# Kernel tuning notes

Hardware: AMD Instinct MI355X
Metric: run time of the kernel (lower is better)

The kernel has to match this reference:

```python
import jax, jax.numpy as jnp
import numpy as np

B, A, F = 8192, 8, 256      # batch, n_agents, per-agent obs feature dim
NA = 16                     # n_actions per agent
H1, H2 = 1024, 1024
OBS_D = A * F               # 2048 flattened obs dim
ACT_D = A * NA              # 128 joint action dim
IN_D = OBS_D + ACT_D        # 2176 MLP input dim


def setup_inputs() -> dict:
    key = jax.random.key(0)
    ks = jax.random.split(key, 8)
    s = 0.02
    return {
        "obs": jax.random.normal(ks[0], (B, A, F), dtype=jnp.float32),
        "all_actions": jax.random.uniform(ks[1], (B, ACT_D), dtype=jnp.float32),
        # per-agent stacked MLP params (agent axis first)
        "W1": jax.random.normal(ks[2], (A, IN_D, H1), dtype=jnp.float32) * s,
        "b1": jnp.zeros((A, H1), dtype=jnp.float32),
        "W2": jax.random.normal(ks[3], (A, H1, H2), dtype=jnp.float32) * s,
        "b2": jnp.zeros((A, H2), dtype=jnp.float32),
        "W3": jax.random.normal(ks[4], (A, H2, NA), dtype=jnp.float32) * s,
        "b3": jnp.zeros((A, NA), dtype=jnp.float32),
    }


def reference(obs, all_actions, W1, b1, W2, b2, W3, b3):
    b_s = obs.shape[0]
    obs_flat = obs.reshape(b_s, OBS_D)                      # [B, A*F]
    # mask[a, g] = 0 on agent a's own action block, 1 elsewhere
    mask = 1.0 - jnp.repeat(jnp.eye(A, dtype=obs.dtype), NA, axis=1)  # [A, A*NA]
    # split W1 into obs / action columns (equivalent to concat-then-dense)
    W1o = W1[:, :OBS_D, :]                                  # [A, OBS_D, H1]
    W1a = W1[:, OBS_D:, :]                                  # [A, ACT_D, H1]
    h1 = jax.nn.relu(
        jnp.einsum("bd,adh->bah", obs_flat, W1o)
        + jnp.einsum("bg,ag,agh->bah", all_actions, mask, W1a)
        + b1
    )                                                        # [B, A, H1]
    h2 = jax.nn.relu(jnp.einsum("bah,ahk->bak", h1, W2) + b2)  # [B, A, H2]
    out = jnp.einsum("bak,akn->ban", h2, W3) + b3              # [B, A, NA]
    return out.reshape(b_s, A * NA)
```

## Files before the change

kernel.cpp:

```cpp
#include <hip/hip_runtime.h>
#include <hip/hip_bf16.h>
#include <cstdint>
#include <cstddef>

typedef __bf16 bf16;
typedef __attribute__((ext_vector_type(8))) __bf16 bf16x8;
typedef __attribute__((ext_vector_type(4))) float f32x4;
typedef __attribute__((ext_vector_type(4))) int i32x4;
typedef __attribute__((address_space(3))) const bf16* lds_cp;

#define B_SZ  8192
#define NAGENT 8
#define NA_N  16
#define OBS_DD 2048
#define ACT_DD 128
#define IN_DD 2176
#define H1_D  1024
#define H2_D  1024

#define BM 256
#define BN 256
#define BK 64
#define GRID_M (B_SZ / BM)
#define GRID_N (1024 / BN)

__device__ __forceinline__ void gload16(const void* g, void* l) {
    __builtin_amdgcn_global_load_lds(
        (__attribute__((address_space(1))) void*)(g),
        (__attribute__((address_space(3))) void*)(l), 16, 0, 0);
}

__global__ void k_prep(const float* __restrict__ obs, const float* __restrict__ act,
                       bf16* __restrict__ xb, const float* __restrict__ b3,
                       float* __restrict__ out, const float* __restrict__ W3,
                       bf16* __restrict__ w3t) {
    const int NX = B_SZ * (IN_DD / 8);
    const int NO = B_SZ * 128 / 4;
    const int NW3 = NAGENT * NA_N * H2_D;
    int idx = blockIdx.x * blockDim.x + threadIdx.x;
    if (idx < NX) {
        const int chunks = IN_DD / 8;
        int b = idx / chunks;
        int c8 = idx - b * chunks;
        const float* src = (c8 < OBS_DD / 8)
            ? (obs + (size_t)b * OBS_DD + c8 * 8)
            : (act + (size_t)b * ACT_DD + (c8 - OBS_DD / 8) * 8);
        float4 v0 = ((const float4*)src)[0];
        float4 v1 = ((const float4*)src)[1];
        bf16x8 o;
        o[0] = (bf16)v0.x; o[1] = (bf16)v0.y; o[2] = (bf16)v0.z; o[3] = (bf16)v0.w;
        o[4] = (bf16)v1.x; o[5] = (bf16)v1.y; o[6] = (bf16)v1.z; o[7] = (bf16)v1.w;
        ((bf16x8*)(xb + (size_t)b * IN_DD))[c8] = o;
    } else if (idx < NX + NO) {
        int i = idx - NX;
        int c = (i & 31) * 4;
        float4 v = make_float4(b3[c], b3[c + 1], b3[c + 2], b3[c + 3]);
        ((float4*)out)[i] = v;
    } else if (idx < NX + NO + NW3) {
        int i = idx - NX - NO;
        int a = i / (NA_N * H2_D);
        int n = (i / H2_D) % NA_N;
        int k = i % H2_D;
        w3t[i] = (bf16)W3[(size_t)a * H2_D * NA_N + (size_t)k * NA_N + n];
    }
}

__global__ void k_transpose_w(const float* __restrict__ src, bf16* __restrict__ dst,
                              int K, int H, int maskStart) {
    __shared__ float tile[32][33];
    int a = blockIdx.z;
    int k0 = blockIdx.x * 32, h0 = blockIdx.y * 32;
    const float* s = src + (size_t)a * K * H;
    bf16* d = dst + (size_t)a * K * H;
    int tx = threadIdx.x, ty = threadIdx.y;
    #pragma unroll
    for (int i = 0; i < 32; i += 8) {
        int k = k0 + ty + i;
        float v = s[(size_t)k * H + h0 + tx];
        if (k >= maskStart) {
            int g = k - maskStart;
            if ((g >> 4) == a) v = 0.f;
        }
        tile[ty + i][tx] = v;
    }
    __syncthreads();
    #pragma unroll
    for (int i = 0; i < 32; i += 8) {
        d[(size_t)(h0 + ty + i) * K + k0 + tx] = (bf16)tile[tx][ty + i];
    }
}

#define DSR4(d0, d1, d2, d3, addr, O0, O1, O2, O3)                      \
    asm volatile("ds_read_b128 %0, %4 offset:" #O0 "\n\t"               \
                 "ds_read_b128 %1, %4 offset:" #O1 "\n\t"               \
                 "ds_read_b128 %2, %4 offset:" #O2 "\n\t"               \
                 "ds_read_b128 %3, %4 offset:" #O3                      \
                 : "=&v"(d0), "=&v"(d1), "=&v"(d2), "=&v"(d3)           \
                 : "v"(addr))

#define BC(x) __builtin_bit_cast(bf16x8, x)

template<int FUSE>
__global__ __launch_bounds__(512, 1)
void k_gemm256(const bf16* __restrict__ Ain, size_t aStride, int lda,
               const bf16* __restrict__ Bw, const float* __restrict__ bias,
               bf16* __restrict__ Cout, size_t cStride, int K,
               int aOff, int nwg, int iters,
               const bf16* __restrict__ W3Tp, float* __restrict__ outp) {
    extern __shared__ bf16 lds[];

    const int tid = threadIdx.x;
    const int w = tid >> 6;
    const int l = tid & 63;

    const int wr = (w >> 2) * 128;
    const int wc = (w & 3) * 64;
    const int lr = l & 15;
    const int lq = l >> 4;

    const int rowA = (wr + lr) * BK;
    const int rowB = (wc + lr) * BK;
    const int ck0 = ((lq ^ (lr & 7)) * 8);
    const int ck1 = (((4 + lq) ^ (lr & 7)) * 8);

    const int sRow = w * 16 + (l >> 3);
    const int sCol = ((l & 7) ^ (l >> 3)) * 8;
    const size_t l8a = (size_t)8 * lda;
    const size_t l8b = (size_t)8 * K;

    const int nkt = K / BK;
    const int q8 = nwg >> 3;

    i32x4 ra0, ra1, ra2, ra3;
    i32x4 rb0, rb1, rb2, rb3;
    i32x4 rc0, rc1, rc2, rc3;
    i32x4 rd0, rd1, rd2, rd3;
    i32x4 re0, re1, re2, re3;
    i32x4 rf0, rf1, rf2, rf3;

#define STAGE_A(t1, half) do {                                              \
        const bf16* g_ = ((half) ? pA1 : pA0) + (t1) * BK;                  \
        bf16* d_ = &lds[(((t1) & 1) * 16384) + (half) * 8192 + w * 1024];   \
        gload16(g_, d_);                                                    \
        gload16(g_ + l8a, d_ + 512);                                        \
    } while (0)
#define STAGE_B(t2, half) do {                                              \
        const bf16* g_ = ((half) ? pB1 : pB0) + (t2) * BK;                  \
        bf16* d_ = &lds[32768 + (((t2) & 1) * 16384) + (half) * 8192 + w * 1024]; \
        gload16(g_, d_);                                                    \
        gload16(g_ + l8b, d_ + 512);                                        \
    } while (0)

#define MFMA16(ACC0, A0, A1, A2, A3, B0, B1, B2, B3)                        \
    do {                                                                    \
        acc[ACC0+0][0] = __builtin_amdgcn_mfma_f32_16x16x32_bf16(BC(A0), BC(B0), acc[ACC0+0][0], 0, 0, 0); \
        acc[ACC0+1][0] = __builtin_amdgcn_mfma_f32_16x16x32_bf16(BC(A1), BC(B0), acc[ACC0+1][0], 0, 0, 0); \
        acc[ACC0+2][0] = __builtin_amdgcn_mfma_f32_16x16x32_bf16(BC(A2), BC(B0), acc[ACC0+2][0], 0, 0, 0); \
        acc[ACC0+3][0] = __builtin_amdgcn_mfma_f32_16x16x32_bf16(BC(A3), BC(B0), acc[ACC0+3][0], 0, 0, 0); \
        acc[ACC0+0][1] = __builtin_amdgcn_mfma_f32_16x16x32_bf16(BC(A0), BC(B1), acc[ACC0+0][1], 0, 0, 0); \
        acc[ACC0+1][1] = __builtin_amdgcn_mfma_f32_16x16x32_bf16(BC(A1), BC(B1), acc[ACC0+1][1], 0, 0, 0); \
        acc[ACC0+2][1] = __builtin_amdgcn_mfma_f32_16x16x32_bf16(BC(A2), BC(B1), acc[ACC0+2][1], 0, 0, 0); \
        acc[ACC0+3][1] = __builtin_amdgcn_mfma_f32_16x16x32_bf16(BC(A3), BC(B1), acc[ACC0+3][1], 0, 0, 0); \
        acc[ACC0+0][2] = __builtin_amdgcn_mfma_f32_16x16x32_bf16(BC(A0), BC(B2), acc[ACC0+0][2], 0, 0, 0); \
        acc[ACC0+1][2] = __builtin_amdgcn_mfma_f32_16x16x32_bf16(BC(A1), BC(B2), acc[ACC0+1][2], 0, 0, 0); \
        acc[ACC0+2][2] = __builtin_amdgcn_mfma_f32_16x16x32_bf16(BC(A2), BC(B2), acc[ACC0+2][2], 0, 0, 0); \
        acc[ACC0+3][2] = __builtin_amdgcn_mfma_f32_16x16x32_bf16(BC(A3), BC(B2), acc[ACC0+3][2], 0, 0, 0); \
        acc[ACC0+0][3] = __builtin_amdgcn_mfma_f32_16x16x32_bf16(BC(A0), BC(B3), acc[ACC0+0][3], 0, 0, 0); \
        acc[ACC0+1][3] = __builtin_amdgcn_mfma_f32_16x16x32_bf16(BC(A1), BC(B3), acc[ACC0+1][3], 0, 0, 0); \
        acc[ACC0+2][3] = __builtin_amdgcn_mfma_f32_16x16x32_bf16(BC(A2), BC(B3), acc[ACC0+2][3], 0, 0, 0); \
        acc[ACC0+3][3] = __builtin_amdgcn_mfma_f32_16x16x32_bf16(BC(A3), BC(B3), acc[ACC0+3][3], 0, 0, 0); \
    } while (0)

    for (int it = 0; it < iters; ++it) {
        const int b = blockIdx.x + gridDim.x * it;
        const int lin2 = (b & 7) * q8 + (b >> 3);
        const int mt = lin2 % GRID_M;
        const int rest = lin2 / GRID_M;
        const int ntile = rest % GRID_N;
        const int az = rest / GRID_N;
        const int aw = az + aOff;

        const int rowBase = mt * BM;
        const int colBase = ntile * BN;
        const bf16* Aag = Ain + (size_t)az * aStride;
        const bf16* Bag = Bw + (size_t)aw * (size_t)1024 * K;

        const bf16* pA0 = Aag + (size_t)(rowBase + sRow) * lda + sCol;
        const bf16* pA1 = Aag + (size_t)(rowBase + 128 + sRow) * lda + sCol;
        const bf16* pB0 = Bag + (size_t)(colBase + sRow) * K + sCol;
        const bf16* pB1 = Bag + (size_t)(colBase + 128 + sRow) * K + sCol;

        f32x4 acc[8][4] = {};

        STAGE_A(0, 0); STAGE_A(0, 1);
        STAGE_B(0, 0); STAGE_B(0, 1);
        asm volatile("s_waitcnt vmcnt(0)" ::: "memory");
        __builtin_amdgcn_s_barrier();

        for (int t = 0; t < nkt; ++t) {
            const int dbuf = (t & 1) * 16384;
            lds_cp adrA0 = (lds_cp)lds + (dbuf + rowA + ck0);
            lds_cp adrA1 = (lds_cp)lds + (dbuf + rowA + ck1);
            lds_cp adrB0 = (lds_cp)lds + (32768 + dbuf + rowB + ck0);
            lds_cp adrB1 = (lds_cp)lds + (32768 + dbuf + rowB + ck1);

            DSR4(ra0, ra1, ra2, ra3, adrA0, 0, 2048, 4096, 6144);
            DSR4(rb0, rb1, rb2, rb3, adrB0, 0, 2048, 4096, 6144);
            DSR4(rc0, rc1, rc2, rc3, adrA0, 8192, 10240, 12288, 14336);
            DSR4(rd0, rd1, rd2, rd3, adrB1, 0, 2048, 4096, 6144);

            if (t + 1 < nkt) {
                STAGE_A(t + 1, 0); STAGE_A(t + 1, 1);
                STAGE_B(t + 1, 0); STAGE_B(t + 1, 1);
            }

            asm volatile("s_waitcnt lgkmcnt(8)" ::: "memory");
            __builtin_amdgcn_sched_barrier(0);
            __builtin_amdgcn_s_setprio(1);
            MFMA16(0, ra0, ra1, ra2, ra3, rb0, rb1, rb2, rb3);
            __builtin_amdgcn_s_setprio(0);

            DSR4(re0, re1, re2, re3, adrA1, 0, 2048, 4096, 6144);
            asm volatile("s_waitcnt lgkmcnt(4)" ::: "memory");
            __builtin_amdgcn_sched_barrier(0);
            __builtin_amdgcn_s_setprio(1);
            MFMA16(4, rc0, rc1, rc2, rc3, rb0, rb1, rb2, rb3);
            __builtin_amdgcn_s_setprio(0);

            DSR4(rf0, rf1, rf2, rf3, adrA1, 8192, 10240, 12288, 14336);
            asm volatile("s_waitcnt lgkmcnt(4)" ::: "memory");
            __builtin_amdgcn_sched_barrier(0);
            __builtin_amdgcn_s_setprio(1);
            MFMA16(0, re0, re1, re2, re3, rd0, rd1, rd2, rd3);
            __builtin_amdgcn_s_setprio(0);

            asm volatile("s_waitcnt vmcnt(0)" ::: "memory");
            asm volatile("s_waitcnt lgkmcnt(0)" ::: "memory");
            __builtin_amdgcn_sched_barrier(0);
            __builtin_amdgcn_s_setprio(1);
            MFMA16(4, rf0, rf1, rf2, rf3, rd0, rd1, rd2, rd3);
            __builtin_amdgcn_s_setprio(0);

            __builtin_amdgcn_s_barrier();
        }

        __syncthreads();
        const float* bAg = bias + (size_t)aw * 1024;
        float bb4[4];
        #pragma unroll
        for (int n = 0; n < 4; ++n) bb4[n] = bAg[colBase + wc + n * 16 + lr];
        #pragma unroll
        for (int m = 0; m < 8; ++m)
            #pragma unroll
            for (int n = 0; n < 4; ++n)
                #pragma unroll
                for (int r = 0; r < 4; ++r) {
                    float v = acc[m][n][r] + bb4[n];
                    v = fmaxf(v, 0.f);
                    int row = wr + m * 16 + lq * 4 + r;
                    int col = wc + n * 16 + lr;
                    lds[row * 256 + ((((col >> 3) ^ (row & 7)) << 3) | (col & 7))] = (bf16)v;
                }
        __syncthreads();

        if constexpr (!FUSE) {
            bf16* Cg = Cout + (size_t)az * cStride + (size_t)rowBase * 1024 + colBase;
            const int er = tid >> 5;
            const int ec = tid & 31;
            #pragma unroll
            for (int i = 0; i < 16; ++i) {
                int row = i * 16 + er;
                int phys = ec ^ (row & 7);
                *(bf16x8*)&Cg[(size_t)row * 1024 + ec * 8] =
                    *(const bf16x8*)&lds[row * 256 + phys * 8];
            }
        } else {
            const bf16* w3a = W3Tp + (size_t)aw * NA_N * H2_D;
            f32x4 oacc[2] = {};
            const int frow0 = w * 32;
            #pragma unroll
            for (int ks = 0; ks < 8; ++ks) {
                bf16x8 bfrag = *(const bf16x8*)&w3a[(size_t)lr * H2_D + colBase + ks * 32 + lq * 8];
                #pragma unroll
                for (int mm = 0; mm < 2; ++mm) {
                    int row = frow0 + mm * 16 + lr;
                    int lc = (ks * 4 + lq) ^ (row & 7);
                    bf16x8 afrag = *(const bf16x8*)&lds[row * 256 + lc * 8];
                    oacc[mm] = __builtin_amdgcn_mfma_f32_16x16x32_bf16(afrag, bfrag, oacc[mm], 0, 0, 0);
                }
            }
            #pragma unroll
            for (int mm = 0; mm < 2; ++mm)
                #pragma unroll
                for (int r = 0; r < 4; ++r)
                    atomicAdd(&outp[(size_t)(rowBase + frow0 + mm * 16 + lq * 4 + r) * 128
                                    + aw * NA_N + lr], oacc[mm][r]);
        }

        __syncthreads();
    }
#undef STAGE_A
#undef STAGE_B
#undef MFMA16
}

extern "C" void kernel_launch(void* const* d_in, const int* in_sizes, int n_in,
                              void* d_out, int out_size, void* d_ws, size_t ws_size,
                              hipStream_t stream) {
    const float* obs = (const float*)d_in[0];
    const float* act = (const float*)d_in[1];
    const float* W1 = (const float*)d_in[2];
    const float* b1 = (const float*)d_in[3];
    const float* W2 = (const float*)d_in[4];
    const float* b2 = (const float*)d_in[5];
    const float* W3 = (const float*)d_in[6];
    const float* b3 = (const float*)d_in[7];
    float* out = (float*)d_out;

    const size_t SZ_XB  = (size_t)B_SZ * IN_DD * 2;
    const size_t SZ_W1T = (size_t)NAGENT * H1_D * IN_DD * 2;
    const size_t SZ_W2T = (size_t)NAGENT * H1_D * H2_D * 2;
    const size_t SZ_W3T = (size_t)NAGENT * NA_N * H2_D * 2;
    const size_t SZ_H1  = (size_t)B_SZ * H1_D * 2;
    const size_t SZ_FIX = SZ_XB + SZ_W1T + SZ_W2T + SZ_W3T;

    char* ws = (char*)d_ws;
    bf16* Xb  = (bf16*)ws;
    bf16* W1T = (bf16*)(ws + SZ_XB);
    bf16* W2T = (bf16*)(ws + SZ_XB + SZ_W1T);
    bf16* W3T = (bf16*)(ws + SZ_XB + SZ_W1T + SZ_W2T);
    char* hbase = ws + SZ_FIX;

    int G = 8;
    while (G > 1 && ws_size < SZ_FIX + (size_t)G * SZ_H1) G >>= 1;

    (void)hipFuncSetAttribute((const void*)k_gemm256<0>,
                              hipFuncAttributeMaxDynamicSharedMemorySize, 131072);
    (void)hipFuncSetAttribute((const void*)k_gemm256<1>,
                              hipFuncAttributeMaxDynamicSharedMemorySize, 131072);

    {
        const int NX = B_SZ * (IN_DD / 8);
        const int NO = B_SZ * 128 / 4;
        const int NW3 = NAGENT * NA_N * H2_D;
        int n = NX + NO + NW3;
        k_prep<<<(n + 255) / 256, 256, 0, stream>>>(obs, act, Xb, b3, out, W3, W3T);
    }
    k_transpose_w<<<dim3(IN_DD / 32, H1_D / 32, NAGENT), dim3(32, 8), 0, stream>>>(
        W1, W1T, IN_DD, H1_D, OBS_DD);
    k_transpose_w<<<dim3(H1_D / 32, H2_D / 32, NAGENT), dim3(32, 8), 0, stream>>>(
        W2, W2T, H1_D, H2_D, 1 << 30);

    const size_t agElems = (size_t)B_SZ * H1_D;
    bf16* h1 = (bf16*)hbase;

    for (int g0 = 0; g0 < NAGENT; g0 += G) {
        const int nwg = 128 * G;
        const int grd = (nwg >= 256) ? 256 : nwg;
        const int iters = nwg / grd;
        k_gemm256<0><<<grd, 512, 131072, stream>>>(
            Xb, 0, IN_DD, W1T, b1, h1, agElems, IN_DD, g0, nwg, iters, nullptr, nullptr);
        k_gemm256<1><<<grd, 512, 131072, stream>>>(
            h1, agElems, H1_D, W2T, b2, nullptr, 0, H1_D, g0, nwg, iters, W3T, out);
    }
    (void)in_sizes; (void)n_in; (void)out_size;
}
```

Measured before the change: 508.2 us.

## Replace persistent GEMM loop with full grid launch and merge weight transposes

The GEMM kernels drop the persistent loop that capped the grid at 256 workgroups, each iterating over several tiles. They now launch one workgroup per output tile on a 3D grid, with the same XCD-aware tile remapping. The two weight-transpose kernels are merged into one launch, with W2 blocks exiting early when past their K range. This trades persistent-block reuse for hardware scheduling of more workgroups and one fewer launch, and adds wasted early-exit blocks in the transpose.

```diff
diff --git a/kernel.cpp b/kernel.cpp
--- a/kernel.cpp
+++ b/kernel.cpp
@@ -61,17 +61,23 @@
         int a = i / (NA_N * H2_D);
         int n = (i / H2_D) % NA_N;
         int k = i % H2_D;
-        w3t[i] = (bf16)W3[(size_t)a * H2_D * NA_N + (size_t)k * NA_N + n];
-    }
-}
-
-__global__ void k_transpose_w(const float* __restrict__ src, bf16* __restrict__ dst,
-                              int K, int H, int maskStart) {
+        w3t[i] = (bf16)W3[(size_t)a * H2_D * NAGENT * 0 + (size_t)a * H2_D * NA_N + (size_t)k * NA_N + n];
+    }
+}
+
+__global__ void k_transpose_w12(const float* __restrict__ W1, bf16* __restrict__ W1T,
+                                const float* __restrict__ W2, bf16* __restrict__ W2T) {
     __shared__ float tile[32][33];
-    int a = blockIdx.z;
+    const int z = blockIdx.z;
+    const bool isW1 = (z < 8);
+    const int a = isW1 ? z : z - 8;
+    const int K = isW1 ? IN_DD : H1_D;
+    const int H = 1024;
+    const int maskStart = isW1 ? OBS_DD : (1 << 30);
+    if (!isW1 && blockIdx.x >= (H1_D / 32)) return;
+    const float* s = (isW1 ? W1 : W2) + (size_t)a * K * H;
+    bf16* d = (isW1 ? W1T : W2T) + (size_t)a * K * H;
     int k0 = blockIdx.x * 32, h0 = blockIdx.y * 32;
-    const float* s = src + (size_t)a * K * H;
-    bf16* d = dst + (size_t)a * K * H;
     int tx = threadIdx.x, ty = threadIdx.y;
     #pragma unroll
     for (int i = 0; i < 32; i += 8) {
@@ -105,13 +111,27 @@
 void k_gemm256(const bf16* __restrict__ Ain, size_t aStride, int lda,
                const bf16* __restrict__ Bw, const float* __restrict__ bias,
                bf16* __restrict__ Cout, size_t cStride, int K,
-               int aOff, int nwg, int iters,
+               int aOff, int gridZ,
                const bf16* __restrict__ W3Tp, float* __restrict__ outp) {
     extern __shared__ bf16 lds[];
 
     const int tid = threadIdx.x;
     const int w = tid >> 6;
     const int l = tid & 63;
+
+    int flat = blockIdx.x + GRID_M * (blockIdx.y + GRID_N * blockIdx.z);
+    int q8 = (GRID_M * GRID_N * gridZ) >> 3;
+    int lin2 = (flat & 7) * q8 + (flat >> 3);
+    const int mt = lin2 % GRID_M;
+    int rest = lin2 / GRID_M;
+    const int ntile = rest % GRID_N;
+    const int az = rest / GRID_N;
+    const int aw = az + aOff;
+
+    const int rowBase = mt * BM;
+    const int colBase = ntile * BN;
+    const bf16* Aag = Ain + (size_t)az * aStride;
+    const bf16* Bag = Bw + (size_t)aw * (size_t)1024 * K;
 
     const int wr = (w >> 2) * 128;
     const int wc = (w & 3) * 64;
@@ -125,18 +145,14 @@
 
     const int sRow = w * 16 + (l >> 3);
     const int sCol = ((l & 7) ^ (l >> 3)) * 8;
+    const bf16* pA0 = Aag + (size_t)(rowBase + sRow) * lda + sCol;
+    const bf16* pA1 = Aag + (size_t)(rowBase + 128 + sRow) * lda + sCol;
+    const bf16* pB0 = Bag + (size_t)(colBase + sRow) * K + sCol;
+    const bf16* pB1 = Bag + (size_t)(colBase + 128 + sRow) * K + sCol;
     const size_t l8a = (size_t)8 * lda;
     const size_t l8b = (size_t)8 * K;
 
     const int nkt = K / BK;
-    const int q8 = nwg >> 3;
-
-    i32x4 ra0, ra1, ra2, ra3;
-    i32x4 rb0, rb1, rb2, rb3;
-    i32x4 rc0, rc1, rc2, rc3;
-    i32x4 rd0, rd1, rd2, rd3;
-    i32x4 re0, re1, re2, re3;
-    i32x4 rf0, rf1, rf2, rf3;
 
 #define STAGE_A(t1, half) do {                                              \
         const bf16* g_ = ((half) ? pA1 : pA0) + (t1) * BK;                  \
@@ -150,6 +166,14 @@
         gload16(g_, d_);                                                    \
         gload16(g_ + l8b, d_ + 512);                                        \
     } while (0)
+
+    f32x4 acc[8][4] = {};
+    i32x4 ra0, ra1, ra2, ra3;
+    i32x4 rb0, rb1, rb2, rb3;
+    i32x4 rc0, rc1, rc2, rc3;
+    i32x4 rd0, rd1, rd2, rd3;
+    i32x4 re0, re1, re2, re3;
+    i32x4 rf0, rf1, rf2, rf3;
 
 #define MFMA16(ACC0, A0, A1, A2, A3, B0, B1, B2, B3)                        \
     do {                                                                    \
@@ -171,137 +195,113 @@
         acc[ACC0+3][3] = __builtin_amdgcn_mfma_f32_16x16x32_bf16(BC(A3), BC(B3), acc[ACC0+3][3], 0, 0, 0); \
     } while (0)
 
-    for (int it = 0; it < iters; ++it) {
-        const int b = blockIdx.x + gridDim.x * it;
-        const int lin2 = (b & 7) * q8 + (b >> 3);
-        const int mt = lin2 % GRID_M;
-        const int rest = lin2 / GRID_M;
-        const int ntile = rest % GRID_N;
-        const int az = rest / GRID_N;
-        const int aw = az + aOff;
-
-        const int rowBase = mt * BM;
-        const int colBase = ntile * BN;
-        const bf16* Aag = Ain + (size_t)az * aStride;
-        const bf16* Bag = Bw + (size_t)aw * (size_t)1024 * K;
-
-        const bf16* pA0 = Aag + (size_t)(rowBase + sRow) * lda + sCol;
-        const bf16* pA1 = Aag + (size_t)(rowBase + 128 + sRow) * lda + sCol;
-        const bf16* pB0 = Bag + (size_t)(colBase + sRow) * K + sCol;
-        const bf16* pB1 = Bag + (size_t)(colBase + 128 + sRow) * K + sCol;
-
-        f32x4 acc[8][4] = {};
-
-        STAGE_A(0, 0); STAGE_A(0, 1);
-        STAGE_B(0, 0); STAGE_B(0, 1);
+    STAGE_A(0, 0); STAGE_A(0, 1);
+    STAGE_B(0, 0); STAGE_B(0, 1);
+    asm volatile("s_waitcnt vmcnt(0)" ::: "memory");
+    __builtin_amdgcn_s_barrier();
+
+    for (int t = 0; t < nkt; ++t) {
+        const int dbuf = (t & 1) * 16384;
+        lds_cp adrA0 = (lds_cp)lds + (dbuf + rowA + ck0);
+        lds_cp adrA1 = (lds_cp)lds + (dbuf + rowA + ck1);
+        lds_cp adrB0 = (lds_cp)lds + (32768 + dbuf + rowB + ck0);
+        lds_cp adrB1 = (lds_cp)lds + (32768 + dbuf + rowB + ck1);
+
+        DSR4(ra0, ra1, ra2, ra3, adrA0, 0, 2048, 4096, 6144);
+        DSR4(rb0, rb1, rb2, rb3, adrB0, 0, 2048, 4096, 6144);
+        DSR4(rc0, rc1, rc2, rc3, adrA0, 8192, 10240, 12288, 14336);
+        DSR4(rd0, rd1, rd2, rd3, adrB1, 0, 2048, 4096, 6144);
+
+        if (t + 1 < nkt) {
+            STAGE_A(t + 1, 0); STAGE_A(t + 1, 1);
+            STAGE_B(t + 1, 0); STAGE_B(t + 1, 1);
+        }
+
+        asm volatile("s_waitcnt lgkmcnt(8)" ::: "memory");
+        __builtin_amdgcn_sched_barrier(0);
+        __builtin_amdgcn_s_setprio(1);
+        MFMA16(0, ra0, ra1, ra2, ra3, rb0, rb1, rb2, rb3);
+        __builtin_amdgcn_s_setprio(0);
+
+        DSR4(re0, re1, re2, re3, adrA1, 0, 2048, 4096, 6144);
+        asm volatile("s_waitcnt lgkmcnt(4)" ::: "memory");
+        __builtin_amdgcn_sched_barrier(0);
+        __builtin_amdgcn_s_setprio(1);
+        MFMA16(4, rc0, rc1, rc2, rc3, rb0, rb1, rb2, rb3);
+        __builtin_amdgcn_s_setprio(0);
+
+        DSR4(rf0, rf1, rf2, rf3, adrA1, 8192, 10240, 12288, 14336);
+        asm volatile("s_waitcnt lgkmcnt(4)" ::: "memory");
+        __builtin_amdgcn_sched_barrier(0);
+        __builtin_amdgcn_s_setprio(1);
+        MFMA16(0, re0, re1, re2, re3, rd0, rd1, rd2, rd3);
+        __builtin_amdgcn_s_setprio(0);
+
         asm volatile("s_waitcnt vmcnt(0)" ::: "memory");
+        asm volatile("s_waitcnt lgkmcnt(0)" ::: "memory");
+        __builtin_amdgcn_sched_barrier(0);
+        __builtin_amdgcn_s_setprio(1);
+        MFMA16(4, rf0, rf1, rf2, rf3, rd0, rd1, rd2, rd3);
+        __builtin_amdgcn_s_setprio(0);
+
         __builtin_amdgcn_s_barrier();
-
-        for (int t = 0; t < nkt; ++t) {
-            const int dbuf = (t & 1) * 16384;
-            lds_cp adrA0 = (lds_cp)lds + (dbuf + rowA + ck0);
-            lds_cp adrA1 = (lds_cp)lds + (dbuf + rowA + ck1);
-            lds_cp adrB0 = (lds_cp)lds + (32768 + dbuf + rowB + ck0);
-            lds_cp adrB1 = (lds_cp)lds + (32768 + dbuf + rowB + ck1);
-
-            DSR4(ra0, ra1, ra2, ra3, adrA0, 0, 2048, 4096, 6144);
-            DSR4(rb0, rb1, rb2, rb3, adrB0, 0, 2048, 4096, 6144);
-            DSR4(rc0, rc1, rc2, rc3, adrA0, 8192, 10240, 12288, 14336);
-            DSR4(rd0, rd1, rd2, rd3, adrB1, 0, 2048, 4096, 6144);
-
-            if (t + 1 < nkt) {
-                STAGE_A(t + 1, 0); STAGE_A(t + 1, 1);
-                STAGE_B(t + 1, 0); STAGE_B(t + 1, 1);
-            }
-
-            asm volatile("s_waitcnt lgkmcnt(8)" ::: "memory");
-            __builtin_amdgcn_sched_barrier(0);
-            __builtin_amdgcn_s_setprio(1);
-            MFMA16(0, ra0, ra1, ra2, ra3, rb0, rb1, rb2, rb3);
-            __builtin_amdgcn_s_setprio(0);
-
-            DSR4(re0, re1, re2, re3, adrA1, 0, 2048, 4096, 6144);
-            asm volatile("s_waitcnt lgkmcnt(4)" ::: "memory");
-            __builtin_amdgcn_sched_barrier(0);
-            __builtin_amdgcn_s_setprio(1);
-            MFMA16(4, rc0, rc1, rc2, rc3, rb0, rb1, rb2, rb3);
-            __builtin_amdgcn_s_setprio(0);
-
-            DSR4(rf0, rf1, rf2, rf3, adrA1, 8192, 10240, 12288, 14336);
-            asm volatile("s_waitcnt lgkmcnt(4)" ::: "memory");
-            __builtin_amdgcn_sched_barrier(0);
-            __builtin_amdgcn_s_setprio(1);
-            MFMA16(0, re0, re1, re2, re3, rd0, rd1, rd2, rd3);
-            __builtin_amdgcn_s_setprio(0);
-
-            asm volatile("s_waitcnt vmcnt(0)" ::: "memory");
-            asm volatile("s_waitcnt lgkmcnt(0)" ::: "memory");
-            __builtin_amdgcn_sched_barrier(0);
-            __builtin_amdgcn_s_setprio(1);
-            MFMA16(4, rf0, rf1, rf2, rf3, rd0, rd1, rd2, rd3);
-            __builtin_amdgcn_s_setprio(0);
-
-            __builtin_amdgcn_s_barrier();
-        }
-
-        __syncthreads();
-        const float* bAg = bias + (size_t)aw * 1024;
-        float bb4[4];
-        #pragma unroll
-        for (int n = 0; n < 4; ++n) bb4[n] = bAg[colBase + wc + n * 16 + lr];
-        #pragma unroll
-        for (int m = 0; m < 8; ++m)
-            #pragma unroll
-            for (int n = 0; n < 4; ++n)
-                #pragma unroll
-                for (int r = 0; r < 4; ++r) {
-                    float v = acc[m][n][r] + bb4[n];
-                    v = fmaxf(v, 0.f);
-                    int row = wr + m * 16 + lq * 4 + r;
-                    int col = wc + n * 16 + lr;
-                    lds[row * 256 + ((((col >> 3) ^ (row & 7)) << 3) | (col & 7))] = (bf16)v;
-                }
-        __syncthreads();
-
-        if constexpr (!FUSE) {
-            bf16* Cg = Cout + (size_t)az * cStride + (size_t)rowBase * 1024 + colBase;
-            const int er = tid >> 5;
-            const int ec = tid & 31;
-            #pragma unroll
-            for (int i = 0; i < 16; ++i) {
-                int row = i * 16 + er;
-                int phys = ec ^ (row & 7);
-                *(bf16x8*)&Cg[(size_t)row * 1024 + ec * 8] =
-                    *(const bf16x8*)&lds[row * 256 + phys * 8];
-            }
-        } else {
-            const bf16* w3a = W3Tp + (size_t)aw * NA_N * H2_D;
-            f32x4 oacc[2] = {};
-            const int frow0 = w * 32;
-            #pragma unroll
-            for (int ks = 0; ks < 8; ++ks) {
-                bf16x8 bfrag = *(const bf16x8*)&w3a[(size_t)lr * H2_D + colBase + ks * 32 + lq * 8];
-                #pragma unroll
-                for (int mm = 0; mm < 2; ++mm) {
-                    int row = frow0 + mm * 16 + lr;
-                    int lc = (ks * 4 + lq) ^ (row & 7);
-                    bf16x8 afrag = *(const bf16x8*)&lds[row * 256 + lc * 8];
-                    oacc[mm] = __builtin_amdgcn_mfma_f32_16x16x32_bf16(afrag, bfrag, oacc[mm], 0, 0, 0);
-                }
-            }
-            #pragma unroll
-            for (int mm = 0; mm < 2; ++mm)
-                #pragma unroll
-                for (int r = 0; r < 4; ++r)
-                    atomicAdd(&outp[(size_t)(rowBase + frow0 + mm * 16 + lq * 4 + r) * 128
-                                    + aw * NA_N + lr], oacc[mm][r]);
-        }
-
-        __syncthreads();
     }
 #undef STAGE_A
 #undef STAGE_B
 #undef MFMA16
+
+    __syncthreads();
+    const float* bAg = bias + (size_t)aw * 1024;
+    float bb4[4];
+    #pragma unroll
+    for (int n = 0; n < 4; ++n) bb4[n] = bAg[colBase + wc + n * 16 + lr];
+    #pragma unroll
+    for (int m = 0; m < 8; ++m)
+        #pragma unroll
+        for (int n = 0; n < 4; ++n)
+            #pragma unroll
+            for (int r = 0; r < 4; ++r) {
+                float v = acc[m][n][r] + bb4[n];
+                v = fmaxf(v, 0.f);
+                int row = wr + m * 16 + lq * 4 + r;
+                int col = wc + n * 16 + lr;
+                lds[row * 256 + ((((col >> 3) ^ (row & 7)) << 3) | (col & 7))] = (bf16)v;
+            }
+    __syncthreads();
+
+    if constexpr (!FUSE) {
+        bf16* Cg = Cout + (size_t)az * cStride + (size_t)rowBase * 1024 + colBase;
+        const int er = tid >> 5;
+        const int ec = tid & 31;
+        #pragma unroll
+        for (int i = 0; i < 16; ++i) {
+            int row = i * 16 + er;
+            int phys = ec ^ (row & 7);
+            *(bf16x8*)&Cg[(size_t)row * 1024 + ec * 8] =
+                *(const bf16x8*)&lds[row * 256 + phys * 8];
+        }
+    } else {
+        const bf16* w3a = W3Tp + (size_t)aw * NA_N * H2_D;
+        f32x4 oacc[2] = {};
+        const int frow0 = w * 32;
+        #pragma unroll
+        for (int ks = 0; ks < 8; ++ks) {
+            bf16x8 bfrag = *(const bf16x8*)&w3a[(size_t)lr * H2_D + colBase + ks * 32 + lq * 8];
+            #pragma unroll
+            for (int mm = 0; mm < 2; ++mm) {
+                int row = frow0 + mm * 16 + lr;
+                int lc = (ks * 4 + lq) ^ (row & 7);
+                bf16x8 afrag = *(const bf16x8*)&lds[row * 256 + lc * 8];
+                oacc[mm] = __builtin_amdgcn_mfma_f32_16x16x32_bf16(afrag, bfrag, oacc[mm], 0, 0, 0);
+            }
+        }
+        #pragma unroll
+        for (int mm = 0; mm < 2; ++mm)
+            #pragma unroll
+            for (int r = 0; r < 4; ++r)
+                atomicAdd(&outp[(size_t)(rowBase + frow0 + mm * 16 + lq * 4 + r) * 128
+                                + aw * NA_N + lr], oacc[mm][r]);
+    }
 }
 
 extern "C" void kernel_launch(void* const* d_in, const int* in_sizes, int n_in,
@@ -346,22 +346,17 @@
         int n = NX + NO + NW3;
         k_prep<<<(n + 255) / 256, 256, 0, stream>>>(obs, act, Xb, b3, out, W3, W3T);
     }
-    k_transpose_w<<<dim3(IN_DD / 32, H1_D / 32, NAGENT), dim3(32, 8), 0, stream>>>(
-        W1, W1T, IN_DD, H1_D, OBS_DD);
-    k_transpose_w<<<dim3(H1_D / 32, H2_D / 32, NAGENT), dim3(32, 8), 0, stream>>>(
-        W2, W2T, H1_D, H2_D, 1 << 30);
+    k_transpose_w12<<<dim3(IN_DD / 32, 1024 / 32, 16), dim3(32, 8), 0, stream>>>(
+        W1, W1T, W2, W2T);
 
     const size_t agElems = (size_t)B_SZ * H1_D;
     bf16* h1 = (bf16*)hbase;
 
     for (int g0 = 0; g0 < NAGENT; g0 += G) {
-        const int nwg = 128 * G;
-        const int grd = (nwg >= 256) ? 256 : nwg;
-        const int iters = nwg / grd;
-        k_gemm256<0><<<grd, 512, 131072, stream>>>(
-            Xb, 0, IN_DD, W1T, b1, h1, agElems, IN_DD, g0, nwg, iters, nullptr, nullptr);
-        k_gemm256<1><<<grd, 512, 131072, stream>>>(
-            h1, agElems, H1_D, W2T, b2, nullptr, 0, H1_D, g0, nwg, iters, W3T, out);
+        k_gemm256<0><<<dim3(GRID_M, GRID_N, G), 512, 131072, stream>>>(
+            Xb, 0, IN_DD, W1T, b1, h1, agElems, IN_DD, g0, G, nullptr, nullptr);
+        k_gemm256<1><<<dim3(GRID_M, GRID_N, G), 512, 131072, stream>>>(
+            h1, agElems, H1_D, W2T, b2, nullptr, 0, H1_D, g0, G, W3T, out);
     }
     (void)in_sizes; (void)n_in; (void)out_size;
 }
```

Result: faster. 441.9 us (-13.0%).
